# Kernel tuning notes

Measured on AMD Instinct MI355X. Metric: run time of the kernel, lower is better.

The kernel has to match this reference:

```python
import jax, jax.numpy as jnp
import numpy as np

N, E, IN_FEATS, H = 20000, 320000, 512, 64
EPS = 1e-5  # BatchNorm eps


def setup_inputs() -> dict:
    key = jax.random.key(0)
    ks = iter(jax.random.split(key, 64))
    rn = lambda *s: jax.random.normal(next(ks), s, dtype=jnp.float32)
    d = {}
    d["x"] = rn(N, IN_FEATS)
    d["edge_index"] = jax.random.randint(next(ks), (2, E), 0, N)
    d["Wm"] = rn(IN_FEATS, H) * 0.05; d["bm"] = rn(H) * 0.05
    d["Wc"] = rn(IN_FEATS, H) * 0.05; d["bc"] = rn(H) * 0.05
    d["Wg1"] = rn(H, 2 * H) * 0.05;     d["bg1"] = rn(2 * H) * 0.05
    d["Wg2"] = rn(2 * H, 2 * H) * 0.05; d["bg2"] = rn(2 * H) * 0.05
    d["Wg3"] = rn(2 * H, 4 * H) * 0.05; d["bg3"] = rn(4 * H) * 0.05
    for name, cin in (("e1", 8 * H), ("e2", 4 * H), ("e3", 4 * H)):
        d[name + "_gamma"] = 1.0 + rn(cin) * 0.1
        d[name + "_beta"] = rn(cin) * 0.1
        d[name + "_mean"] = rn(cin) * 0.1
        d[name + "_var"] = jax.random.uniform(next(ks), (cin,), dtype=jnp.float32) + 0.5
        d[name + "_W"] = rn(cin, 2 * H) * 0.05
    d["Wfc"] = rn(2 * H, 1) * 0.05; d["bfc"] = rn(1) * 0.05
    return d


def _gcn(x, W, b, src, dst, n):
    """PyG GCNConv: self-loops + symmetric normalization + sum aggregation."""
    h = x @ W  # [N, out]
    loop = jnp.arange(n)
    s = jnp.concatenate([src, loop])
    d = jnp.concatenate([dst, loop])
    deg = jax.ops.segment_sum(jnp.ones(s.shape[0], h.dtype), d, num_segments=n)
    dinv = jnp.where(deg > 0, jax.lax.rsqrt(deg), 0.0)
    msg = h[s] * (dinv[s] * dinv[d])[:, None]  # gather + normalize
    return jax.ops.segment_sum(msg, d, num_segments=n) + b


def _edge_conv(x, gamma, beta, mean, var, W, src, dst, n):
    """PyG EdgeConv with LinearPathPreact nn (BN->ReLU->Linear), max aggregation."""
    xi = x[dst]
    xj = x[src]
    feat = jnp.concatenate([xi, xj - xi], axis=-1)  # [E, 2*C]
    h = (feat - mean) * jax.lax.rsqrt(var + EPS) * gamma + beta  # BN (eval stats)
    h = jnp.maximum(h, 0.0) @ W  # ReLU -> Linear(bias=False)
    out = jax.ops.segment_max(h, dst, num_segments=n)
    return jnp.where(jnp.isfinite(out), out, 0.0)  # empty segments -> 0


def reference(x, edge_index, Wm, bm, Wc, bc, Wg1, bg1, Wg2, bg2, Wg3, bg3,
              e1_gamma, e1_beta, e1_mean, e1_var, e1_W,
              e2_gamma, e2_beta, e2_mean, e2_var, e2_W,
              e3_gamma, e3_beta, e3_mean, e3_var, e3_W,
              Wfc, bfc):
    n = x.shape[0]
    src, dst = edge_index[0], edge_index[1]
    x0_main = x @ Wm + bm
    x0 = x @ Wc + bc
    x0 = x0.at[0::4].set(x0_main[0::4])  # main-person rows use the main projection
    g = _gcn(x0, Wg1, bg1, src, dst, n)
    g = _gcn(g, Wg2, bg2, src, dst, n)
    g = _gcn(g, Wg3, bg3, src, dst, n)
    h = _edge_conv(g, e1_gamma, e1_beta, e1_mean, e1_var, e1_W, src, dst, n)
    h = _edge_conv(h, e2_gamma, e2_beta, e2_mean, e2_var, e2_W, src, dst, n)
    h = _edge_conv(h, e3_gamma, e3_beta, e3_mean, e3_var, e3_W, src, dst, n)
    return h @ Wfc + bfc  # [N, 1]
```

## Files before the change

kernel.cpp:

```cpp
#include <hip/hip_runtime.h>

#define DEVINL __device__ __forceinline__

constexpr int N_NODES  = 20000;
constexpr int N_EDGES  = 320000;
constexpr int IN_FEATS = 512;

static_assert(N_EDGES % 128 == 0, "edge tiling assumes E % 128 == 0");
static_assert(N_NODES % 16 == 0, "proj assumes N % 16 == 0");

typedef __attribute__((ext_vector_type(8))) short short8;
typedef __attribute__((ext_vector_type(4))) float f32x4;

DEVINL unsigned enc_f32(float v) {
  unsigned b = __float_as_uint(v);
  return (b & 0x80000000u) ? ~b : (b | 0x80000000u);
}
DEVINL float dec_f32(unsigned e) {
  unsigned b = (e & 0x80000000u) ? (e & 0x7FFFFFFFu) : ~e;
  return __uint_as_float(b);
}

DEVINL unsigned short bf16_rne(float f) {
  unsigned u = __float_as_uint(f);
  u += 0x7FFFu + ((u >> 16) & 1u);
  return (unsigned short)(u >> 16);
}
DEVINL void split_bf16(float v, unsigned short& h, unsigned short& l) {
  h = bf16_rne(v);
  float hf = __uint_as_float((unsigned)h << 16);
  l = bf16_rne(v - hf);
}

DEVINL void glds16(const unsigned short* g, unsigned short* l) {
  __builtin_amdgcn_global_load_lds(
      (const __attribute__((address_space(1))) unsigned int*)g,
      (__attribute__((address_space(3))) unsigned int*)l, 16, 0, 0);
}

__global__ void hist_kernel(const int* __restrict__ dst, int* __restrict__ cnt, int e) {
  int i = blockIdx.x * 256 + threadIdx.x;
  if (i < e) atomicAdd(&cnt[dst[i]], 1);
}
__global__ void dinv_kernel(const int* __restrict__ cnt, float* __restrict__ dinv,
                            float* __restrict__ dinv2, int n) {
  int i = blockIdx.x * 256 + threadIdx.x;
  if (i < n) {
    float s = rsqrtf((float)cnt[i] + 1.0f);
    dinv[i] = s;
    dinv2[i] = s * s;
  }
}
__global__ void __launch_bounds__(256)
scan_p1(const int* __restrict__ cnt, int* __restrict__ rp, int* __restrict__ bsum, int n) {
  __shared__ int buf[256];
  int i = blockIdx.x * 256 + threadIdx.x;
  int v = (i < n) ? cnt[i] : 0;
  buf[threadIdx.x] = v;
  __syncthreads();
  for (int off = 1; off < 256; off <<= 1) {
    int t = (threadIdx.x >= off) ? buf[threadIdx.x - off] : 0;
    __syncthreads();
    buf[threadIdx.x] += t;
    __syncthreads();
  }
  if (i < n) rp[i] = buf[threadIdx.x] - v;
  if (threadIdx.x == 255) bsum[blockIdx.x] = buf[255];
}
__global__ void __launch_bounds__(256)
scan_p2(int* __restrict__ bsum, int nb) {
  __shared__ int buf[256];
  int v = (threadIdx.x < nb) ? bsum[threadIdx.x] : 0;
  buf[threadIdx.x] = v;
  __syncthreads();
  for (int off = 1; off < 256; off <<= 1) {
    int t = (threadIdx.x >= off) ? buf[threadIdx.x - off] : 0;
    __syncthreads();
    buf[threadIdx.x] += t;
    __syncthreads();
  }
  if (threadIdx.x < nb) bsum[threadIdx.x] = buf[threadIdx.x] - v;
}
__global__ void __launch_bounds__(256)
scan_p3(int* __restrict__ rp, const int* __restrict__ bsum, int* __restrict__ cursor,
        int n, int e) {
  int i = blockIdx.x * 256 + threadIdx.x;
  if (i < n) {
    int v = rp[i] + bsum[blockIdx.x];
    rp[i] = v;
    cursor[i] = v;
  }
  if (i == 0) rp[n] = e;
}
__global__ void scatter_edges_kernel(const int* __restrict__ src, const int* __restrict__ dst,
                                     int* __restrict__ cursor, int* __restrict__ ssrc,
                                     int* __restrict__ sdst, int e) {
  int i = blockIdx.x * 256 + threadIdx.x;
  if (i < e) {
    int d = dst[i];
    int pos = atomicAdd(&cursor[d], 1);
    ssrc[pos] = src[i];
    sdst[pos] = d;
  }
}

__global__ void uvec1_kernel(const int* __restrict__ row_ptr, const int* __restrict__ ssrc,
                             const float* __restrict__ dinv, float* __restrict__ u1,
                             float* __restrict__ w1, int n) {
  int d = blockIdx.x * 256 + threadIdx.x;
  if (d >= n) return;
  float s = dinv[d];
  float acc = s;
  int e = row_ptr[d], end = row_ptr[d + 1];
  for (; e < end; ++e) acc += dinv[ssrc[e]];
  float u = s * acc;
  u1[d] = u;
  w1[d] = s * u;
}
__global__ void uvec2_kernel(const int* __restrict__ row_ptr, const int* __restrict__ ssrc,
                             const float* __restrict__ dinv, const float* __restrict__ w1,
                             float* __restrict__ u2, int n) {
  int d = blockIdx.x * 256 + threadIdx.x;
  if (d >= n) return;
  float acc = w1[d];
  int e = row_ptr[d], end = row_ptr[d + 1];
  for (; e < end; ++e) acc += w1[ssrc[e]];
  u2[d] = dinv[d] * acc;
}

__global__ void smallmm(const float* __restrict__ A, const float* __restrict__ B,
                        float* __restrict__ Cc, int m, int k, int n) {
  int i = blockIdx.x * 256 + threadIdx.x;
  if (i >= m * n) return;
  int r = i / n, c = i % n;
  float acc = 0.f;
  for (int kk = 0; kk < k; ++kk) acc = fmaf(A[r * k + kk], B[kk * n + c], acc);
  Cc[i] = acc;
}

DEVINL void bn1(const float* g, const float* b, const float* m, const float* v,
                float* sc, float* sh, int i) {
  float s = g[i] * rsqrtf(v[i] + 1e-5f);
  sc[i] = s;
  sh[i] = b[i] - m[i] * s;
}
__global__ void bn_prep_all(const float* g1, const float* b1, const float* m1, const float* v1,
                            float* sc1, float* sh1, const float* g2, const float* b2,
                            const float* m2, const float* v2, float* sc2, float* sh2,
                            const float* g3, const float* b3, const float* m3, const float* v3,
                            float* sc3, float* sh3) {
  int i = blockIdx.x * 256 + threadIdx.x;
  if (i < 512) bn1(g1, b1, m1, v1, sc1, sh1, i);
  else if (i < 768) bn1(g2, b2, m2, v2, sc2, sh2, i - 512);
  else if (i < 1024) bn1(g3, b3, m3, v3, sc3, sh3, i - 768);
}

DEVINL void wfrag1(const float* W, unsigned short* out, int e) {
  int k = e >> 7, c = e & 127;
  unsigned short h, l;
  split_bf16(W[e], h, l);
  int chunk = k >> 5, kq = (k >> 3) & 3, j = k & 7, ct = c >> 4, n = c & 15;
  int frag = (ct * 4 + kq) * 16 + n;
  size_t o = (size_t)chunk * 8192 + frag * 8 + j;
  out[o] = h;
  out[o + 4096] = l;
}
__global__ void wfrag_all(const float* __restrict__ e1W, const float* __restrict__ e2W,
                          const float* __restrict__ e3W, unsigned short* b1p,
                          unsigned short* b1q, unsigned short* b2p, unsigned short* b2q,
                          unsigned short* b3p, unsigned short* b3q) {
  int g = blockIdx.x * 256 + threadIdx.x;
  if (g < 32768) wfrag1(e1W, b1p, g);
  else if (g < 65536) wfrag1(e1W + 32768, b1q, g - 32768);
  else if (g < 81920) wfrag1(e2W, b2p, g - 65536);
  else if (g < 98304) wfrag1(e2W + 16384, b2q, g - 81920);
  else if (g < 114688) wfrag1(e3W, b3p, g - 98304);
  else wfrag1(e3W + 16384, b3q, g - 114688);
}

__global__ void combine_kernel(unsigned* __restrict__ Q, const float* __restrict__ P,
                               float* __restrict__ H, int n, int zq) {
  int i = blockIdx.x * 256 + threadIdx.x;
  if (i < n) {
    unsigned e = Q[i];
    H[i] = e ? (P[i] + dec_f32(e)) : 0.f;
    if (zq) Q[i] = 0u;
  }
}

__global__ void __launch_bounds__(256)
proj_kernel(const float* __restrict__ X, const float* __restrict__ Wm,
            const float* __restrict__ bm, const float* __restrict__ Wc,
            const float* __restrict__ bc, const float* __restrict__ dinv,
            float* __restrict__ Y0) {
  __shared__ float xs[16][IN_FEATS];
  int tid = threadIdx.x;
  int rowBase = blockIdx.x * 16;
  for (int i = 0; i < 8; ++i) {
    int idx = i * 256 + tid;
    int r = idx >> 7, kq = idx & 127;
    *reinterpret_cast<float4*>(&xs[r][kq * 4]) =
        *reinterpret_cast<const float4*>(X + (size_t)(rowBase + r) * IN_FEATS + kq * 4);
  }
  __syncthreads();
  int r4 = tid >> 6;
  int j = tid & 63;
  const float* W = (r4 == 0) ? Wm : Wc;
  float a0 = 0.f, a1 = 0.f, a2 = 0.f, a3 = 0.f;
#pragma unroll 4
  for (int k = 0; k < IN_FEATS; ++k) {
    float w = W[k * 64 + j];
    a0 = fmaf(xs[r4][k], w, a0);
    a1 = fmaf(xs[r4 + 4][k], w, a1);
    a2 = fmaf(xs[r4 + 8][k], w, a2);
    a3 = fmaf(xs[r4 + 12][k], w, a3);
  }
  float b = (r4 == 0) ? bm[j] : bc[j];
  int r0 = rowBase + r4;
  Y0[(size_t)r0 * 64 + j] = (a0 + b) * dinv[r0];
  Y0[(size_t)(r0 + 4) * 64 + j] = (a1 + b) * dinv[r0 + 4];
  Y0[(size_t)(r0 + 8) * 64 + j] = (a2 + b) * dinv[r0 + 8];
  Y0[(size_t)(r0 + 12) * 64 + j] = (a3 + b) * dinv[r0 + 12];
}

template <int LOGF4>
__global__ void __launch_bounds__(256)
agg_kernel(const float* __restrict__ Y, const int* __restrict__ row_ptr,
           const int* __restrict__ ssrc, const float* __restrict__ mfac,
           float* __restrict__ Z, int n) {
  constexpr int F4 = 1 << LOGF4;
  int g = blockIdx.x * 256 + threadIdx.x;
  int d = g >> LOGF4, c4 = g & (F4 - 1);
  if (d >= n) return;
  const float4* Yp = (const float4*)Y;
  float4 a = Yp[(size_t)d * F4 + c4];
  float ax = a.x, ay = a.y, az = a.z, aw = a.w;
  int e = row_ptr[d], end = row_ptr[d + 1];
  for (; e + 7 < end; e += 8) {
    int s[8];
#pragma unroll
    for (int i = 0; i < 8; ++i) s[i] = ssrc[e + i];
    float4 v[8];
#pragma unroll
    for (int i = 0; i < 8; ++i) v[i] = Yp[(size_t)s[i] * F4 + c4];
#pragma unroll
    for (int i = 0; i < 8; ++i) {
      ax += v[i].x; ay += v[i].y; az += v[i].z; aw += v[i].w;
    }
  }
  for (; e < end; ++e) {
    float4 v = Yp[(size_t)ssrc[e] * F4 + c4];
    ax += v.x; ay += v.y; az += v.z; aw += v.w;
  }
  float s = mfac[d];
  ((float4*)Z)[(size_t)d * F4 + c4] = make_float4(ax * s, ay * s, az * s, aw * s);
}

__global__ void __launch_bounds__(256)
gemm_rank1_kernel(const float* __restrict__ X, const float* __restrict__ W,
                  const float* __restrict__ b3, const float* __restrict__ u1,
                  const float* __restrict__ u2, const float* __restrict__ c1,
                  const float* __restrict__ c2, float* __restrict__ H, int n) {
  constexpr int K = 64, F = 256;
  __shared__ float Xs[64][K + 1];
  __shared__ float Ws[K][65];
  int tid = threadIdx.x;
  int rowBase = blockIdx.x * 64;
  int colBase = blockIdx.y * 64;
  for (int idx = tid; idx < 64 * K; idx += 256) {
    int r = idx / K, k = idx % K;
    int row = rowBase + r;
    Xs[r][k] = (row < n) ? X[(size_t)row * K + k] : 0.f;
  }
  for (int idx = tid; idx < K * 64; idx += 256) {
    int k = idx >> 6, c = idx & 63;
    Ws[k][c] = W[(size_t)k * F + colBase + c];
  }
  __syncthreads();
  int tx = tid & 15, ty = tid >> 4;
  float acc[4][4] = {};
  for (int k = 0; k < K; ++k) {
    float a[4], b[4];
#pragma unroll
    for (int r = 0; r < 4; ++r) a[r] = Xs[ty * 4 + r][k];
#pragma unroll
    for (int c = 0; c < 4; ++c) b[c] = Ws[k][tx * 4 + c];
#pragma unroll
    for (int r = 0; r < 4; ++r)
#pragma unroll
      for (int c = 0; c < 4; ++c) acc[r][c] = fmaf(a[r], b[c], acc[r][c]);
  }
#pragma unroll
  for (int r = 0; r < 4; ++r) {
    int row = rowBase + ty * 4 + r;
    if (row < n) {
      float du2 = u2[row], du1 = u1[row];
#pragma unroll
      for (int c = 0; c < 4; ++c) {
        int col = colBase + tx * 4 + c;
        float v = acc[r][c] + du2 * c1[col] + du1 * c2[col] + b3[col];
        H[(size_t)row * F + col] = v;
      }
    }
  }
}

DEVINL void proc8(const float4& va, const float4& vb, const float4& sa, const float4& sb,
                  const float4& ha, const float4& hb, short8& hi, short8& lo) {
  float f[8] = {va.x, va.y, va.z, va.w, vb.x, vb.y, vb.z, vb.w};
  float s[8] = {sa.x, sa.y, sa.z, sa.w, sb.x, sb.y, sb.z, sb.w};
  float t[8] = {ha.x, ha.y, ha.z, ha.w, hb.x, hb.y, hb.z, hb.w};
#pragma unroll
  for (int j = 0; j < 8; ++j) {
    float v = fmaxf(fmaf(f[j], s[j], t[j]), 0.f);
    unsigned short hh, ll;
    split_bf16(v, hh, ll);
    hi[j] = (short)hh;
    lo[j] = (short)ll;
  }
}

template <int C, bool EDGE>
__global__ void __launch_bounds__(256, 2)
ec_mfma_kernel(const float* __restrict__ X, const int* __restrict__ ssrc,
               const int* __restrict__ sdst, const float* __restrict__ scale,
               const float* __restrict__ shift, const unsigned short* __restrict__ Bfrag,
               unsigned* __restrict__ outU, float* __restrict__ outP, int nrows) {
  constexpr int NCH = C / 32;
  constexpr int HALVES = C / 128;
  __shared__ unsigned short Bmat[32768];
  __shared__ float ss[2 * C];
  __shared__ int de_s[128];
  const int tid = threadIdx.x, lane = tid & 63, wv = tid >> 6;
  const int q = lane >> 4, mn = lane & 15;
  const int base = blockIdx.x * 128;
  const int koff = q * 8;
  const int lr0 = wv * 32 + mn, lr1 = lr0 + 16;

  int id0, id1, is0 = 0, is1 = 0;
  if (EDGE) {
    if (tid < 128) de_s[tid] = sdst[base + tid];
    is0 = ssrc[base + lr0];
    id0 = sdst[base + lr0];
    is1 = ssrc[base + lr1];
    id1 = sdst[base + lr1];
  } else {
    id0 = min(base + lr0, nrows - 1);
    id1 = min(base + lr1, nrows - 1);
  }
  const float* pd0 = X + (size_t)id0 * C + koff;
  const float* pd1 = X + (size_t)id1 * C + koff;
  const float* ps0 = EDGE ? X + (size_t)is0 * C + koff : nullptr;
  const float* ps1 = EDGE ? X + (size_t)is1 * C + koff : nullptr;

  f32x4 acc[8][2];
#pragma unroll
  for (int i = 0; i < 8; ++i) {
    acc[i][0] = (f32x4)0.f;
    acc[i][1] = (f32x4)0.f;
  }

  float4 A[3][8];
#define LOAD_A(cc, slot)                                   \
  {                                                        \
    const int kk_ = (cc) * 32;                             \
    A[slot][0] = *(const float4*)(pd0 + kk_);              \
    A[slot][1] = *(const float4*)(pd0 + kk_ + 4);          \
    A[slot][2] = *(const float4*)(pd1 + kk_);              \
    A[slot][3] = *(const float4*)(pd1 + kk_ + 4);          \
    if (EDGE) {                                            \
      A[slot][4] = *(const float4*)(ps0 + kk_);            \
      A[slot][5] = *(const float4*)(ps0 + kk_ + 4);        \
      A[slot][6] = *(const float4*)(ps1 + kk_);            \
      A[slot][7] = *(const float4*)(ps1 + kk_ + 4);        \
    }                                                      \
  }

  LOAD_A(0, 0);
  if (NCH > 1) LOAD_A(1, 1);
  {
    constexpr int NF4 = C / 4;
    if (tid < NF4)
      ((float4*)ss)[tid] = ((const float4*)scale)[tid];
    else if (tid < 2 * NF4)
      ((float4*)(ss + C))[tid - NF4] = ((const float4*)shift)[tid - NF4];
  }
  {
    const unsigned short* bs = Bfrag + lane * 8;
#pragma unroll
    for (int i = 0; i < 16; ++i) {
      int seg = wv * 16 + i;
      glds16(bs + seg * 512, Bmat + seg * 512);
    }
  }
  __syncthreads();

#pragma unroll
  for (int h = 0; h < HALVES; ++h) {
    if (h > 0) {
      __syncthreads();
      const unsigned short* bs = Bfrag + 32768 + lane * 8;
#pragma unroll
      for (int i = 0; i < 16; ++i) {
        int seg = wv * 16 + i;
        glds16(bs + seg * 512, Bmat + seg * 512);
      }
      __syncthreads();
    }
#pragma unroll
    for (int cc = 0; cc < 4; ++cc) {
      const int c = h * 4 + cc;
      const int kc = c * 32;
      if (c + 2 < NCH) LOAD_A(c + 2, (c + 2) % 3);
      float4 sca = *(const float4*)&ss[kc + koff];
      float4 scb = *(const float4*)&ss[kc + koff + 4];
      float4 sha = *(const float4*)&ss[C + kc + koff];
      float4 shb = *(const float4*)&ss[C + kc + koff + 4];
      const int sl = c % 3;
      float4 u0, u1, u2, u3;
      if (EDGE) {
        u0 = make_float4(A[sl][4].x - A[sl][0].x, A[sl][4].y - A[sl][0].y,
                         A[sl][4].z - A[sl][0].z, A[sl][4].w - A[sl][0].w);
        u1 = make_float4(A[sl][5].x - A[sl][1].x, A[sl][5].y - A[sl][1].y,
                         A[sl][5].z - A[sl][1].z, A[sl][5].w - A[sl][1].w);
        u2 = make_float4(A[sl][6].x - A[sl][2].x, A[sl][6].y - A[sl][2].y,
                         A[sl][6].z - A[sl][2].z, A[sl][6].w - A[sl][2].w);
        u3 = make_float4(A[sl][7].x - A[sl][3].x, A[sl][7].y - A[sl][3].y,
                         A[sl][7].z - A[sl][3].z, A[sl][7].w - A[sl][3].w);
      } else {
        u0 = A[sl][0]; u1 = A[sl][1]; u2 = A[sl][2]; u3 = A[sl][3];
      }
      short8 ah0, al0, ah1, al1;
      proc8(u0, u1, sca, scb, sha, shb, ah0, al0);
      proc8(u2, u3, sca, scb, sha, shb, ah1, al1);
      const unsigned short* Bc = Bmat + cc * 8192;
#pragma unroll
      for (int ct = 0; ct < 8; ++ct) {
        int fi = ct * 64 + lane;
        short8 bh = *(const short8*)(Bc + fi * 8);
        short8 bl = *(const short8*)(Bc + 4096 + fi * 8);
        acc[ct][0] = __builtin_amdgcn_mfma_f32_16x16x32_bf16(ah0, bh, acc[ct][0], 0, 0, 0);
        acc[ct][1] = __builtin_amdgcn_mfma_f32_16x16x32_bf16(ah1, bh, acc[ct][1], 0, 0, 0);
        acc[ct][0] = __builtin_amdgcn_mfma_f32_16x16x32_bf16(ah0, bl, acc[ct][0], 0, 0, 0);
        acc[ct][1] = __builtin_amdgcn_mfma_f32_16x16x32_bf16(ah1, bl, acc[ct][1], 0, 0, 0);
        acc[ct][0] = __builtin_amdgcn_mfma_f32_16x16x32_bf16(al0, bh, acc[ct][0], 0, 0, 0);
        acc[ct][1] = __builtin_amdgcn_mfma_f32_16x16x32_bf16(al1, bh, acc[ct][1], 0, 0, 0);
      }
    }
  }
#undef LOAD_A

  if (EDGE) {
#pragma unroll
    for (int ct = 0; ct < 8; ++ct) {
      int f = ct * 16 + mn;
      float mv = 0.f;
      int prev = -1;
#pragma unroll
      for (int g = 0; g < 2; ++g) {
        int e0 = wv * 32 + g * 16 + q * 4;
#pragma unroll
        for (int r = 0; r < 4; ++r) {
          int d = de_s[e0 + r];
          float v = acc[ct][g][r];
          if (prev < 0) {
            prev = d; mv = v;
          } else if (d == prev) {
            mv = fmaxf(mv, v);
          } else {
            atomicMax(&outU[(size_t)prev * 128 + f], enc_f32(mv));
            prev = d; mv = v;
          }
        }
      }
      atomicMax(&outU[(size_t)prev * 128 + f], enc_f32(mv));
    }
  } else {
#pragma unroll
    for (int ct = 0; ct < 8; ++ct) {
      int f = ct * 16 + mn;
#pragma unroll
      for (int g = 0; g < 2; ++g) {
        int r0 = base + wv * 32 + g * 16 + q * 4;
#pragma unroll
        for (int r = 0; r < 4; ++r) {
          int row = r0 + r;
          if (row < nrows) outP[(size_t)row * 128 + f] = acc[ct][g][r];
        }
      }
    }
  }
}

__global__ void __launch_bounds__(256)
fc_kernel(const float* __restrict__ Hf, const float* __restrict__ Wfc,
          const float* __restrict__ bfc, float* __restrict__ out, int n) {
  int g = blockIdx.x * 256 + threadIdx.x;
  int node = g >> 6, lane = g & 63;
  if (node >= n) return;
  float v = fmaf(Hf[(size_t)node * 128 + lane], Wfc[lane],
                 Hf[(size_t)node * 128 + 64 + lane] * Wfc[64 + lane]);
#pragma unroll
  for (int off = 32; off > 0; off >>= 1) v += __shfl_down(v, off);
  if (lane == 0) out[node] = v + bfc[0];
}

extern "C" void kernel_launch(void* const* d_in, const int* in_sizes, int n_in,
                              void* d_out, int out_size, void* d_ws, size_t ws_size,
                              hipStream_t stream) {
  const float* x   = (const float*)d_in[0];
  const int*   ei  = (const int*)d_in[1];
  const float* Wm  = (const float*)d_in[2];
  const float* bm  = (const float*)d_in[3];
  const float* Wc  = (const float*)d_in[4];
  const float* bc  = (const float*)d_in[5];
  const float* Wg1 = (const float*)d_in[6];
  const float* bg1 = (const float*)d_in[7];
  const float* Wg2 = (const float*)d_in[8];
  const float* bg2 = (const float*)d_in[9];
  const float* Wg3 = (const float*)d_in[10];
  const float* bg3 = (const float*)d_in[11];
  const float* e1g = (const float*)d_in[12];
  const float* e1b = (const float*)d_in[13];
  const float* e1m = (const float*)d_in[14];
  const float* e1v = (const float*)d_in[15];
  const float* e1W = (const float*)d_in[16];
  const float* e2g = (const float*)d_in[17];
  const float* e2b = (const float*)d_in[18];
  const float* e2m = (const float*)d_in[19];
  const float* e2v = (const float*)d_in[20];
  const float* e2W = (const float*)d_in[21];
  const float* e3g = (const float*)d_in[22];
  const float* e3b = (const float*)d_in[23];
  const float* e3m = (const float*)d_in[24];
  const float* e3v = (const float*)d_in[25];
  const float* e3W = (const float*)d_in[26];
  const float* Wfc = (const float*)d_in[27];
  const float* bfc = (const float*)d_in[28];

  const int* src = ei;
  const int* dst = ei + N_EDGES;

  float* ws    = (float*)d_ws;
  float* dinv  = ws;
  float* dinv2 = dinv + N_NODES;
  float* u1    = dinv2 + N_NODES;
  float* w1    = u1 + N_NODES;
  float* u2    = w1 + N_NODES;
  float* y0    = u2 + N_NODES;
  float* za    = y0 + (size_t)N_NODES * 64;
  float* zb    = za + (size_t)N_NODES * 64;
  float* PQ    = zb + (size_t)N_NODES * 64;
  float* G     = PQ + (size_t)N_NODES * 256;
  float* sc1   = G + (size_t)N_NODES * 256;
  float* sh1   = sc1 + 512;
  float* sc2   = sh1 + 512;
  float* sh2   = sc2 + 256;
  float* sc3   = sh2 + 256;
  float* sh3   = sc3 + 256;
  unsigned short* bf1p = (unsigned short*)(sh3 + 256);
  unsigned short* bf1q = bf1p + 65536;
  unsigned short* bf2p = bf1q + 65536;
  unsigned short* bf2q = bf2p + 32768;
  unsigned short* bf3p = bf2q + 32768;
  unsigned short* bf3q = bf3p + 32768;
  float* W23   = (float*)(bf3q + 32768);
  float* W123  = W23 + 32768;
  float* c1    = W123 + 16384;
  float* c2    = c1 + 256;
  int* cnt     = (int*)(c2 + 256);
  int* row_ptr = cnt + N_NODES;
  int* cursor  = row_ptr + N_NODES + 1;
  int* bsum    = cursor + N_NODES;
  int* ssrc    = bsum + 256;
  int* sdst    = ssrc + N_EDGES;

  float*    Pbuf = PQ;
  unsigned* Qbuf = (unsigned*)(PQ + (size_t)N_NODES * 128);

  hipMemsetAsync(cnt, 0, N_NODES * sizeof(int), stream);
  hist_kernel<<<N_EDGES / 256, 256, 0, stream>>>(dst, cnt, N_EDGES);
  dinv_kernel<<<79, 256, 0, stream>>>(cnt, dinv, dinv2, N_NODES);
  scan_p1<<<79, 256, 0, stream>>>(cnt, row_ptr, bsum, N_NODES);
  scan_p2<<<1, 256, 0, stream>>>(bsum, 79);
  scan_p3<<<79, 256, 0, stream>>>(row_ptr, bsum, cursor, N_NODES, N_EDGES);
  scatter_edges_kernel<<<N_EDGES / 256, 256, 0, stream>>>(src, dst, cursor, ssrc, sdst,
                                                          N_EDGES);

  smallmm<<<128, 256, 0, stream>>>(Wg2, Wg3, W23, 128, 128, 256);
  smallmm<<<64, 256, 0, stream>>>(Wg1, W23, W123, 64, 128, 256);
  smallmm<<<1, 256, 0, stream>>>(bg1, W23, c1, 1, 128, 256);
  smallmm<<<1, 256, 0, stream>>>(bg2, Wg3, c2, 1, 128, 256);
  uvec1_kernel<<<79, 256, 0, stream>>>(row_ptr, ssrc, dinv, u1, w1, N_NODES);
  uvec2_kernel<<<79, 256, 0, stream>>>(row_ptr, ssrc, dinv, w1, u2, N_NODES);

  bn_prep_all<<<4, 256, 0, stream>>>(e1g, e1b, e1m, e1v, sc1, sh1, e2g, e2b, e2m, e2v, sc2,
                                     sh2, e3g, e3b, e3m, e3v, sc3, sh3);
  wfrag_all<<<512, 256, 0, stream>>>(e1W, e2W, e3W, bf1p, bf1q, bf2p, bf2q, bf3p, bf3q);

  proj_kernel<<<N_NODES / 16, 256, 0, stream>>>(x, Wm, bm, Wc, bc, dinv, y0);
  agg_kernel<4><<<N_NODES * 16 / 256, 256, 0, stream>>>(y0, row_ptr, ssrc, dinv2, za, N_NODES);
  agg_kernel<4><<<N_NODES * 16 / 256, 256, 0, stream>>>(za, row_ptr, ssrc, dinv2, zb, N_NODES);
  agg_kernel<4><<<N_NODES * 16 / 256, 256, 0, stream>>>(zb, row_ptr, ssrc, dinv, za, N_NODES);
  dim3 grid4(313, 4);
  gemm_rank1_kernel<<<grid4, 256, 0, stream>>>(za, W123, bg3, u1, u2, c1, c2, G, N_NODES);

  const int NODE_BLOCKS = (N_NODES + 127) / 128;
  const int EDGE_BLOCKS = N_EDGES / 128;
  const int NB_ELEM     = N_NODES * 128 / 256;

  float* H1 = G;
  float* H2 = G + (size_t)N_NODES * 128;
  float* H3 = G;

  hipMemsetAsync(Qbuf, 0, (size_t)N_NODES * 128 * 4, stream);
  ec_mfma_kernel<256, false><<<NODE_BLOCKS, 256, 0, stream>>>(
      G, nullptr, nullptr, sc1, sh1, bf1p, nullptr, Pbuf, N_NODES);
  ec_mfma_kernel<256, true><<<EDGE_BLOCKS, 256, 0, stream>>>(
      G, ssrc, sdst, sc1 + 256, sh1 + 256, bf1q, Qbuf, nullptr, N_NODES);
  combine_kernel<<<NB_ELEM, 256, 0, stream>>>(Qbuf, Pbuf, H1, N_NODES * 128, 1);

  ec_mfma_kernel<128, false><<<NODE_BLOCKS, 256, 0, stream>>>(
      H1, nullptr, nullptr, sc2, sh2, bf2p, nullptr, Pbuf, N_NODES);
  ec_mfma_kernel<128, true><<<EDGE_BLOCKS, 256, 0, stream>>>(
      H1, ssrc, sdst, sc2 + 128, sh2 + 128, bf2q, Qbuf, nullptr, N_NODES);
  combine_kernel<<<NB_ELEM, 256, 0, stream>>>(Qbuf, Pbuf, H2, N_NODES * 128, 1);

  ec_mfma_kernel<128, false><<<NODE_BLOCKS, 256, 0, stream>>>(
      H2, nullptr, nullptr, sc3, sh3, bf3p, nullptr, Pbuf, N_NODES);
  ec_mfma_kernel<128, true><<<EDGE_BLOCKS, 256, 0, stream>>>(
      H2, ssrc, sdst, sc3 + 128, sh3 + 128, bf3q, Qbuf, nullptr, N_NODES);
  combine_kernel<<<NB_ELEM, 256, 0, stream>>>(Qbuf, Pbuf, H3, N_NODES * 128, 0);

  fc_kernel<<<N_NODES * 64 / 256, 256, 0, stream>>>(H3, Wfc, bfc, (float*)d_out, N_NODES);
}
```

Baseline: 802.4 us.

## Merge edge and node EdgeConv passes into one launch with 64-row tiles

Result: faster. 710.3 us (-11.5%).

```diff
diff --git a/kernel.cpp b/kernel.cpp
--- a/kernel.cpp
+++ b/kernel.cpp
@@ -6,7 +6,7 @@
 constexpr int N_EDGES  = 320000;
 constexpr int IN_FEATS = 512;
 
-static_assert(N_EDGES % 128 == 0, "edge tiling assumes E % 128 == 0");
+static_assert(N_EDGES % 64 == 0, "edge tiling assumes E % 64 == 0");
 static_assert(N_NODES % 16 == 0, "proj assumes N % 16 == 0");
 
 typedef __attribute__((ext_vector_type(8))) short short8;
@@ -128,14 +128,26 @@
   u2[d] = dinv[d] * acc;
 }
 
-__global__ void smallmm(const float* __restrict__ A, const float* __restrict__ B,
-                        float* __restrict__ Cc, int m, int k, int n) {
-  int i = blockIdx.x * 256 + threadIdx.x;
-  if (i >= m * n) return;
-  int r = i / n, c = i % n;
-  float acc = 0.f;
-  for (int kk = 0; kk < k; ++kk) acc = fmaf(A[r * k + kk], B[kk * n + c], acc);
-  Cc[i] = acc;
+__global__ void smallmm2(const float* __restrict__ A1, const float* __restrict__ B1,
+                         float* __restrict__ C1, int m1, int k1, int n1,
+                         const float* __restrict__ A2, const float* __restrict__ B2,
+                         float* __restrict__ C2, int m2, int k2, int n2) {
+  int i = blockIdx.x * 256 + threadIdx.x;
+  int t1 = m1 * n1;
+  if (i < t1) {
+    int r = i / n1, c = i % n1;
+    float acc = 0.f;
+    for (int kk = 0; kk < k1; ++kk) acc = fmaf(A1[r * k1 + kk], B1[kk * n1 + c], acc);
+    C1[i] = acc;
+  } else {
+    i -= t1;
+    if (i < m2 * n2) {
+      int r = i / n2, c = i % n2;
+      float acc = 0.f;
+      for (int kk = 0; kk < k2; ++kk) acc = fmaf(A2[r * k2 + kk], B2[kk * n2 + c], acc);
+      C2[i] = acc;
+    }
+  }
 }
 
 DEVINL void bn1(const float* g, const float* b, const float* m, const float* v,
@@ -179,12 +191,12 @@
 }
 
 __global__ void combine_kernel(unsigned* __restrict__ Q, const float* __restrict__ P,
-                               float* __restrict__ H, int n, int zq) {
+                               float* __restrict__ H, int n) {
   int i = blockIdx.x * 256 + threadIdx.x;
   if (i < n) {
     unsigned e = Q[i];
     H[i] = e ? (P[i] + dec_f32(e)) : 0.f;
-    if (zq) Q[i] = 0u;
+    Q[i] = 0u;
   }
 }
 
@@ -320,64 +332,60 @@
   }
 }
 
-template <int C, bool EDGE>
-__global__ void __launch_bounds__(256, 2)
+template <int C>
+__global__ void __launch_bounds__(256, 4)
 ec_mfma_kernel(const float* __restrict__ X, const int* __restrict__ ssrc,
-               const int* __restrict__ sdst, const float* __restrict__ scale,
-               const float* __restrict__ shift, const unsigned short* __restrict__ Bfrag,
-               unsigned* __restrict__ outU, float* __restrict__ outP, int nrows) {
+               const int* __restrict__ sdst,
+               const float* __restrict__ scaleQ, const float* __restrict__ shiftQ,
+               const unsigned short* __restrict__ BfragQ,
+               const float* __restrict__ scaleP, const float* __restrict__ shiftP,
+               const unsigned short* __restrict__ BfragP,
+               unsigned* __restrict__ outU, float* __restrict__ outP,
+               int nrows, int edge_blocks) {
   constexpr int NCH = C / 32;
-  constexpr int HALVES = C / 128;
-  __shared__ unsigned short Bmat[32768];
+  constexpr int NSTAGE = NCH / 2;
+  __shared__ unsigned short Bmat[16384];
   __shared__ float ss[2 * C];
-  __shared__ int de_s[128];
+  __shared__ int de_s[64];
   const int tid = threadIdx.x, lane = tid & 63, wv = tid >> 6;
   const int q = lane >> 4, mn = lane & 15;
-  const int base = blockIdx.x * 128;
+  const bool EDGE = (int)blockIdx.x < edge_blocks;
+  const int base = (EDGE ? (int)blockIdx.x : (int)blockIdx.x - edge_blocks) * 64;
   const int koff = q * 8;
-  const int lr0 = wv * 32 + mn, lr1 = lr0 + 16;
-
-  int id0, id1, is0 = 0, is1 = 0;
+  const int lr = wv * 16 + mn;
+
+  const float* scale = EDGE ? scaleQ : scaleP;
+  const float* shift = EDGE ? shiftQ : shiftP;
+  const unsigned short* Bfrag = EDGE ? BfragQ : BfragP;
+
+  int id, is = 0;
   if (EDGE) {
-    if (tid < 128) de_s[tid] = sdst[base + tid];
-    is0 = ssrc[base + lr0];
-    id0 = sdst[base + lr0];
-    is1 = ssrc[base + lr1];
-    id1 = sdst[base + lr1];
+    if (tid < 64) de_s[tid] = sdst[base + tid];
+    is = ssrc[base + lr];
+    id = sdst[base + lr];
   } else {
-    id0 = min(base + lr0, nrows - 1);
-    id1 = min(base + lr1, nrows - 1);
-  }
-  const float* pd0 = X + (size_t)id0 * C + koff;
-  const float* pd1 = X + (size_t)id1 * C + koff;
-  const float* ps0 = EDGE ? X + (size_t)is0 * C + koff : nullptr;
-  const float* ps1 = EDGE ? X + (size_t)is1 * C + koff : nullptr;
-
-  f32x4 acc[8][2];
-#pragma unroll
-  for (int i = 0; i < 8; ++i) {
-    acc[i][0] = (f32x4)0.f;
-    acc[i][1] = (f32x4)0.f;
-  }
-
-  float4 A[3][8];
-#define LOAD_A(cc, slot)                                   \
-  {                                                        \
-    const int kk_ = (cc) * 32;                             \
-    A[slot][0] = *(const float4*)(pd0 + kk_);              \
-    A[slot][1] = *(const float4*)(pd0 + kk_ + 4);          \
-    A[slot][2] = *(const float4*)(pd1 + kk_);              \
-    A[slot][3] = *(const float4*)(pd1 + kk_ + 4);          \
-    if (EDGE) {                                            \
-      A[slot][4] = *(const float4*)(ps0 + kk_);            \
-      A[slot][5] = *(const float4*)(ps0 + kk_ + 4);        \
-      A[slot][6] = *(const float4*)(ps1 + kk_);            \
-      A[slot][7] = *(const float4*)(ps1 + kk_ + 4);        \
-    }                                                      \
+    id = min(base + lr, nrows - 1);
+  }
+  const float* pd = X + (size_t)id * C + koff;
+  const float* ps = EDGE ? X + (size_t)is * C + koff : nullptr;
+
+  f32x4 acc[8];
+#pragma unroll
+  for (int i = 0; i < 8; ++i) acc[i] = (f32x4)0.f;
+
+  float4 A[2][4];
+#define LOAD_A(cc, slot)                              \
+  {                                                   \
+    const int kk_ = (cc) * 32;                        \
+    A[slot][0] = *(const float4*)(pd + kk_);          \
+    A[slot][1] = *(const float4*)(pd + kk_ + 4);      \
+    if (EDGE) {                                       \
+      A[slot][2] = *(const float4*)(ps + kk_);        \
+      A[slot][3] = *(const float4*)(ps + kk_ + 4);    \
+    }                                                 \
   }
 
   LOAD_A(0, 0);
-  if (NCH > 1) LOAD_A(1, 1);
   {
     constexpr int NF4 = C / 4;
     if (tid < NF4)
@@ -388,118 +396,107 @@
   {
     const unsigned short* bs = Bfrag + lane * 8;
 #pragma unroll
-    for (int i = 0; i < 16; ++i) {
-      int seg = wv * 16 + i;
+    for (int i = 0; i < 8; ++i) {
+      int seg = wv * 8 + i;
       glds16(bs + seg * 512, Bmat + seg * 512);
     }
   }
-  __syncthreads();
-
-#pragma unroll
-  for (int h = 0; h < HALVES; ++h) {
-    if (h > 0) {
+
+#pragma unroll
+  for (int s = 0; s < NSTAGE; ++s) {
+    if (s > 0) {
       __syncthreads();
-      const unsigned short* bs = Bfrag + 32768 + lane * 8;
-#pragma unroll
-      for (int i = 0; i < 16; ++i) {
-        int seg = wv * 16 + i;
+      const unsigned short* bs = Bfrag + (size_t)s * 16384 + lane * 8;
+#pragma unroll
+      for (int i = 0; i < 8; ++i) {
+        int seg = wv * 8 + i;
         glds16(bs + seg * 512, Bmat + seg * 512);
       }
-      __syncthreads();
-    }
-#pragma unroll
-    for (int cc = 0; cc < 4; ++cc) {
-      const int c = h * 4 + cc;
+    }
+    __syncthreads();
+#pragma unroll
+    for (int cc = 0; cc < 2; ++cc) {
+      const int c = s * 2 + cc;
       const int kc = c * 32;
-      if (c + 2 < NCH) LOAD_A(c + 2, (c + 2) % 3);
+      if (c + 1 < NCH) LOAD_A(c + 1, (c + 1) & 1);
       float4 sca = *(const float4*)&ss[kc + koff];
       float4 scb = *(const float4*)&ss[kc + koff + 4];
       float4 sha = *(const float4*)&ss[C + kc + koff];
       float4 shb = *(const float4*)&ss[C + kc + koff + 4];
-      const int sl = c % 3;
-      float4 u0, u1, u2, u3;
+      const int sl = c & 1;
+      float4 u0, u1;
       if (EDGE) {
-        u0 = make_float4(A[sl][4].x - A[sl][0].x, A[sl][4].y - A[sl][0].y,
-                         A[sl][4].z - A[sl][0].z, A[sl][4].w - A[sl][0].w);
-        u1 = make_float4(A[sl][5].x - A[sl][1].x, A[sl][5].y - A[sl][1].y,
-                         A[sl][5].z - A[sl][1].z, A[sl][5].w - A[sl][1].w);
-        u2 = make_float4(A[sl][6].x - A[sl][2].x, A[sl][6].y - A[sl][2].y,
-                         A[sl][6].z - A[sl][2].z, A[sl][6].w - A[sl][2].w);
-        u3 = make_float4(A[sl][7].x - A[sl][3].x, A[sl][7].y - A[sl][3].y,
-                         A[sl][7].z - A[sl][3].z, A[sl][7].w - A[sl][3].w);
+        u0 = make_float4(A[sl][2].x - A[sl][0].x, A[sl][2].y - A[sl][0].y,
+                         A[sl][2].z - A[sl][0].z, A[sl][2].w - A[sl][0].w);
+        u1 = make_float4(A[sl][3].x - A[sl][1].x, A[sl][3].y - A[sl][1].y,
+                         A[sl][3].z - A[sl][1].z, A[sl][3].w - A[sl][1].w);
       } else {
-        u0 = A[sl][0]; u1 = A[sl][1]; u2 = A[sl][2]; u3 = A[sl][3];
+        u0 = A[sl][0];
+        u1 = A[sl][1];
       }
-      short8 ah0, al0, ah1, al1;
-      proc8(u0, u1, sca, scb, sha, shb, ah0, al0);
-      proc8(u2, u3, sca, scb, sha, shb, ah1, al1);
+      short8 ah, al;
+      proc8(u0, u1, sca, scb, sha, shb, ah, al);
       const unsigned short* Bc = Bmat + cc * 8192;
 #pragma unroll
       for (int ct = 0; ct < 8; ++ct) {
         int fi = ct * 64 + lane;
         short8 bh = *(const short8*)(Bc + fi * 8);
         short8 bl = *(const short8*)(Bc + 4096 + fi * 8);
-        acc[ct][0] = __builtin_amdgcn_mfma_f32_16x16x32_bf16(ah0, bh, acc[ct][0], 0, 0, 0);
-        acc[ct][1] = __builtin_amdgcn_mfma_f32_16x16x32_bf16(ah1, bh, acc[ct][1], 0, 0, 0);
-        acc[ct][0] = __builtin_amdgcn_mfma_f32_16x16x32_bf16(ah0, bl, acc[ct][0], 0, 0, 0);
-        acc[ct][1] = __builtin_amdgcn_mfma_f32_16x16x32_bf16(ah1, bl, acc[ct][1], 0, 0, 0);
-        acc[ct][0] = __builtin_amdgcn_mfma_f32_16x16x32_bf16(al0, bh, acc[ct][0], 0, 0, 0);
-        acc[ct][1] = __builtin_amdgcn_mfma_f32_16x16x32_bf16(al1, bh, acc[ct][1], 0, 0, 0);
+        acc[ct] = __builtin_amdgcn_mfma_f32_16x16x32_bf16(ah, bh, acc[ct], 0, 0, 0);
+        acc[ct] = __builtin_amdgcn_mfma_f32_16x16x32_bf16(ah, bl, acc[ct], 0, 0, 0);
+        acc[ct] = __builtin_amdgcn_mfma_f32_16x16x32_bf16(al, bh, acc[ct], 0, 0, 0);
       }
     }
   }
 #undef LOAD_A
 
   if (EDGE) {
+    int e0 = wv * 16 + q * 4;
 #pragma unroll
     for (int ct = 0; ct < 8; ++ct) {
       int f = ct * 16 + mn;
-      float mv = 0.f;
-      int prev = -1;
-#pragma unroll
-      for (int g = 0; g < 2; ++g) {
-        int e0 = wv * 32 + g * 16 + q * 4;
-#pragma unroll
-        for (int r = 0; r < 4; ++r) {
-          int d = de_s[e0 + r];
-          float v = acc[ct][g][r];
-          if (prev < 0) {
-            prev = d; mv = v;
-          } else if (d == prev) {
-            mv = fmaxf(mv, v);
-          } else {
-            atomicMax(&outU[(size_t)prev * 128 + f], enc_f32(mv));
-            prev = d; mv = v;
-          }
+      int prev = de_s[e0];
+      float mv = acc[ct][0];
+#pragma unroll
+      for (int r = 1; r < 4; ++r) {
+        int d = de_s[e0 + r];
+        float v = acc[ct][r];
+        if (d == prev) {
+          mv = fmaxf(mv, v);
+        } else {
+          atomicMax(&outU[(size_t)prev * 128 + f], enc_f32(mv));
+          prev = d;
+          mv = v;
         }
       }
       atomicMax(&outU[(size_t)prev * 128 + f], enc_f32(mv));
     }
   } else {
+    int r0 = base + wv * 16 + q * 4;
 #pragma unroll
     for (int ct = 0; ct < 8; ++ct) {
       int f = ct * 16 + mn;
 #pragma unroll
-      for (int g = 0; g < 2; ++g) {
-        int r0 = base + wv * 32 + g * 16 + q * 4;
-#pragma unroll
-        for (int r = 0; r < 4; ++r) {
-          int row = r0 + r;
-          if (row < nrows) outP[(size_t)row * 128 + f] = acc[ct][g][r];
-        }
+      for (int r = 0; r < 4; ++r) {
+        int row = r0 + r;
+        if (row < nrows) outP[(size_t)row * 128 + f] = acc[ct][r];
       }
     }
   }
 }
 
 __global__ void __launch_bounds__(256)
-fc_kernel(const float* __restrict__ Hf, const float* __restrict__ Wfc,
-          const float* __restrict__ bfc, float* __restrict__ out, int n) {
+fc_kernel(const unsigned* __restrict__ Q, const float* __restrict__ P,
+          const float* __restrict__ Wfc, const float* __restrict__ bfc,
+          float* __restrict__ out, int n) {
   int g = blockIdx.x * 256 + threadIdx.x;
   int node = g >> 6, lane = g & 63;
   if (node >= n) return;
-  float v = fmaf(Hf[(size_t)node * 128 + lane], Wfc[lane],
-                 Hf[(size_t)node * 128 + 64 + lane] * Wfc[64 + lane]);
+  size_t b = (size_t)node * 128;
+  unsigned q0 = Q[b + lane], q1 = Q[b + 64 + lane];
+  float h0 = q0 ? (P[b + lane] + dec_f32(q0)) : 0.f;
+  float h1 = q1 ? (P[b + 64 + lane] + dec_f32(q1)) : 0.f;
+  float v = fmaf(h0, Wfc[lane], h1 * Wfc[64 + lane]);
 #pragma unroll
   for (int off = 32; off > 0; off >>= 1) v += __shfl_down(v, off);
   if (lane == 0) out[node] = v + bfc[0];
@@ -587,10 +584,10 @@
   scatter_edges_kernel<<<N_EDGES / 256, 256, 0, stream>>>(src, dst, cursor, ssrc, sdst,
                                                           N_EDGES);
 
-  smallmm<<<128, 256, 0, stream>>>(Wg2, Wg3, W23, 128, 128, 256);
-  smallmm<<<64, 256, 0, stream>>>(Wg1, W23, W123, 64, 128, 256);
-  smallmm<<<1, 256, 0, stream>>>(bg1, W23, c1, 1, 128, 256);
-  smallmm<<<1, 256, 0, stream>>>(bg2, Wg3, c2, 1, 128, 256);
+  smallmm2<<<129, 256, 0, stream>>>(Wg2, Wg3, W23, 128, 128, 256,
+                                    bg2, Wg3, c2, 1, 128, 256);
+  smallmm2<<<65, 256, 0, stream>>>(Wg1, W23, W123, 64, 128, 256,
+                                   bg1, W23, c1, 1, 128, 256);
   uvec1_kernel<<<79, 256, 0, stream>>>(row_ptr, ssrc, dinv, u1, w1, N_NODES);
   uvec2_kernel<<<79, 256, 0, stream>>>(row_ptr, ssrc, dinv, w1, u2, N_NODES);
 
@@ -605,32 +602,28 @@
   dim3 grid4(313, 4);
   gemm_rank1_kernel<<<grid4, 256, 0, stream>>>(za, W123, bg3, u1, u2, c1, c2, G, N_NODES);
 
-  const int NODE_BLOCKS = (N_NODES + 127) / 128;
-  const int EDGE_BLOCKS = N_EDGES / 128;
+  const int EDGE_BLOCKS = N_EDGES / 64;
+  const int NODE_BLOCKS = (N_NODES + 63) / 64;
+  const int EC_BLOCKS   = EDGE_BLOCKS + NODE_BLOCKS;
   const int NB_ELEM     = N_NODES * 128 / 256;
 
   float* H1 = G;
   float* H2 = G + (size_t)N_NODES * 128;
-  float* H3 = G;
 
   hipMemsetAsync(Qbuf, 0, (size_t)N_NODES * 128 * 4, stream);
-  ec_mfma_kernel<256, false><<<NODE_BLOCKS, 256, 0, stream>>>(
-      G, nullptr, nullptr, sc1, sh1, bf1p, nullptr, Pbuf, N_NODES);
-  ec_mfma_kernel<256, true><<<EDGE_BLOCKS, 256, 0, stream>>>(
-      G, ssrc, sdst, sc1 + 256, sh1 + 256, bf1q, Qbuf, nullptr, N_NODES);
-  combine_kernel<<<NB_ELEM, 256, 0, stream>>>(Qbuf, Pbuf, H1, N_NODES * 128, 1);
-
-  ec_mfma_kernel<128, false><<<NODE_BLOCKS, 256, 0, stream>>>(
-      H1, nullptr, nullptr, sc2, sh2, bf2p, nullptr, Pbuf, N_NODES);
-  ec_mfma_kernel<128, true><<<EDGE_BLOCKS, 256, 0, stream>>>(
-      H1, ssrc, sdst, sc2 + 128, sh2 + 128, bf2q, Qbuf, nullptr, N_NODES);
-  combine_kernel<<<NB_ELEM, 256, 0, stream>>>(Qbuf, Pbuf, H2, N_NODES * 128, 1);
-
-  ec_mfma_kernel<128, false><<<NODE_BLOCKS, 256, 0, stream>>>(
-      H2, nullptr, nullptr, sc3, sh3, bf3p, nullptr, Pbuf, N_NODES);
-  ec_mfma_kernel<128, true><<<EDGE_BLOCKS, 256, 0, stream>>>(
-      H2, ssrc, sdst, sc3 + 128, sh3 + 128, bf3q, Qbuf, nullptr, N_NODES);
-  combine_kernel<<<NB_ELEM, 256, 0, stream>>>(Qbuf, Pbuf, H3, N_NODES * 128, 0);
-
-  fc_kernel<<<N_NODES * 64 / 256, 256, 0, stream>>>(H3, Wfc, bfc, (float*)d_out, N_NODES);
-}
+  ec_mfma_kernel<256><<<EC_BLOCKS, 256, 0, stream>>>(
+      G, ssrc, sdst, sc1 + 256, sh1 + 256, bf1q, sc1, sh1, bf1p, Qbuf, Pbuf, N_NODES,
+      EDGE_BLOCKS);
+  combine_kernel<<<NB_ELEM, 256, 0, stream>>>(Qbuf, Pbuf, H1, N_NODES * 128);
+
+  ec_mfma_kernel<128><<<EC_BLOCKS, 256, 0, stream>>>(
+      H1, ssrc, sdst, sc2 + 128, sh2 + 128, bf2q, sc2, sh2, bf2p, Qbuf, Pbuf, N_NODES,
+      EDGE_BLOCKS);
+  combine_kernel<<<NB_ELEM, 256, 0, stream>>>(Qbuf, Pbuf, H2, N_NODES * 128);
+
+  ec_mfma_kernel<128><<<EC_BLOCKS, 256, 0, stream>>>(
+      H2, ssrc, sdst, sc3 + 128, sh3 + 128, bf3q, sc3, sh3, bf3p, Qbuf, Pbuf, N_NODES,
+      EDGE_BLOCKS);
+  fc_kernel<<<N_NODES * 64 / 256, 256, 0, stream>>>(Qbuf, Pbuf, Wfc, bfc, (float*)d_out,
+                                                    N_NODES);
+}
```
